# Performance work log

Hardware: AMD Instinct MI355X
Metric: run time of the kernel (lower is better)

## Reference

```python
import jax, jax.numpy as jnp
import numpy as np

H = 128        # hidden_channels
R = 32         # num_rbf
L = 2          # num_layers
CUTOFF = 4.5   # cutoff_upper (cutoff_lower = 0)
N_ATOMS = 2048
N_EDGES = 32768


def _tensor_norm(t):
    # Frobenius norm squared over the trailing 3x3 -> [N, H]
    return jnp.sum(t * t, axis=(-2, -1))


def _decompose(t):
    # Split into isotropic (I), antisymmetric (A), traceless symmetric (S) parts.
    eye = jnp.eye(3, dtype=t.dtype)
    I = (jnp.trace(t, axis1=-2, axis2=-1) / 3.0)[..., None, None] * eye
    A = 0.5 * (t - jnp.swapaxes(t, -2, -1))
    S = 0.5 * (t + jnp.swapaxes(t, -2, -1)) - I
    return I, A, S


def _chan_mix(T, W):
    # torch nn.Linear(H, H, bias=False) applied on the channel axis of [N,H,3,3]
    return jnp.einsum('nhij,gh->ngij', T, W)


def _interaction(X, edge_index, edge_weight, edge_attr, q,
                 W1, b1, W2, b2, W3, b3, Wt):
    N = X.shape[0]
    src, dst = edge_index[0], edge_index[1]
    # cosine cutoff (cutoff_lower = 0)
    C = 0.5 * (jnp.cos(edge_weight * (jnp.pi / CUTOFF)) + 1.0)
    C = C * (edge_weight < CUTOFF).astype(C.dtype)
    # edge scalar MLP: R -> H -> 2H -> 3H, silu
    ea = jax.nn.silu(edge_attr @ W1.T + b1)
    ea = jax.nn.silu(ea @ W2.T + b2)
    ea = jax.nn.silu(ea @ W3.T + b3)
    ea = (ea * C[:, None]).reshape(-1, H, 3)       # [E, H, 3]
    # normalize node tensors
    X = X / (_tensor_norm(X) + 1.0)[..., None, None]
    I, A, S = _decompose(X)
    I = _chan_mix(I, Wt[0])
    A = _chan_mix(A, Wt[1])
    S = _chan_mix(S, Wt[2])
    Y = I + A + S
    # per-edge tensor messages (Im + Am + Sm fused before the scatter)
    msg = (ea[:, :, 0, None, None] * I[dst]
           + ea[:, :, 1, None, None] * A[dst]
           + ea[:, :, 2, None, None] * S[dst])   # [E, H, 3, 3]
    M = jax.ops.segment_sum(msg, src, num_segments=N)
    # O(3) group: symmetrized tensor product, scaled by charge factor
    AB = jnp.matmul(M, Y) + jnp.matmul(Y, M)
    I, A, S = _decompose((1.0 + 0.1 * q[:, None, None, None]) * AB)
    normp1 = (_tensor_norm(I + A + S) + 1.0)[..., None, None]
    I, A, S = I / normp1, A / normp1, S / normp1
    I = _chan_mix(I, Wt[3])
    A = _chan_mix(A, Wt[4])
    S = _chan_mix(S, Wt[5])
    dX = I + A + S
    return X + dX + (1.0 + 0.1 * q[:, None, None, None]) * jnp.matmul(dX, dX)


def setup_inputs() -> dict:
    key = jax.random.key(0)
    ks = jax.random.split(key, 10)
    N, E = N_ATOMS, N_EDGES
    X = jax.random.normal(ks[0], (N, H, 3, 3), jnp.float32)
    edge_index = jax.random.randint(ks[1], (2, E), 0, N, jnp.int32)
    edge_weight = jax.random.uniform(ks[2], (E,), jnp.float32, 0.1, CUTOFF)
    edge_attr = jax.random.normal(ks[3], (E, R), jnp.float32)
    q = jax.random.normal(ks[4], (N,), jnp.float32) * 0.1
    s = 0.05
    Ws1 = jax.random.normal(ks[5], (L, H, R), jnp.float32) * s
    bs1 = jnp.zeros((L, H), jnp.float32)
    Ws2 = jax.random.normal(ks[6], (L, 2 * H, H), jnp.float32) * s
    bs2 = jnp.zeros((L, 2 * H), jnp.float32)
    Ws3 = jax.random.normal(ks[7], (L, 3 * H, 2 * H), jnp.float32) * s
    bs3 = jnp.zeros((L, 3 * H), jnp.float32)
    Wt = jax.random.normal(ks[8], (L, 6, H, H), jnp.float32) * s
    return dict(X=X, edge_attr=edge_attr, edge_weight=edge_weight, q=q,
                Ws1=Ws1, bs1=bs1, Ws2=Ws2, bs2=bs2, Ws3=Ws3, bs3=bs3,
                Wt=Wt, edge_index=edge_index)


def reference(X, edge_attr, edge_weight, q, Ws1, bs1, Ws2, bs2, Ws3, bs3, Wt, edge_index):
    for l in range(L):
        X = _interaction(X, edge_index, edge_weight, edge_attr, q,
                         Ws1[l], bs1[l], Ws2[l], bs2[l], Ws3[l], bs3[l], Wt[l])
    return X
```

## Files before the change

### kernel.cpp

```cpp
#include <hip/hip_runtime.h>
#include <hip/hip_bf16.h>
#include <math.h>

#define H 128
#define R 32
#define NATOMS 2048
#define NEDGES 32768
#define NH (NATOMS * H)
#define NP 1152
#define CUTOFF_F 4.5f
#define PI_OVER_CUTOFF 0.6981317007977318f

typedef __bf16 bf16x8 __attribute__((ext_vector_type(8)));
typedef float f32x4 __attribute__((ext_vector_type(4)));
typedef short short8 __attribute__((ext_vector_type(8)));

__device__ __forceinline__ float silu_f(float x) {
    return x / (1.f + __expf(-x));
}
__device__ __forceinline__ float b2f(unsigned short u) {
    return __uint_as_float(((unsigned)u) << 16);
}
__device__ __forceinline__ unsigned short f2b(float f) {
    __hip_bfloat16 h = __float2bfloat16(f);
    return __builtin_bit_cast(unsigned short, h);
}

__device__ __forceinline__ void build_full(const float d[9], float m[9]) {
    float i0 = d[0], a01 = d[1], a02 = d[2], a12 = d[3];
    float s00 = d[4], s01 = d[5], s02 = d[6], s11 = d[7], s12 = d[8];
    float s22 = -(s00 + s11);
    m[0] = i0 + s00;  m[1] = a01 + s01;  m[2] = a02 + s02;
    m[3] = s01 - a01; m[4] = i0 + s11;   m[5] = a12 + s12;
    m[6] = s02 - a02; m[7] = s12 - a12;  m[8] = i0 + s22;
}

#define C0 (NEDGES * R)
#define C1 (2 * H * R)
#define C2 (2 * 2 * H * H)
#define C3 (2 * 3 * H * 2 * H)
#define C4 (2 * 6 * H * H)
__global__ __launch_bounds__(256) void k_cast_all(
        const float* __restrict__ ea, const float* __restrict__ w1,
        const float* __restrict__ w2, const float* __restrict__ w3,
        const float* __restrict__ wt,
        __hip_bfloat16* __restrict__ oea, __hip_bfloat16* __restrict__ ow1,
        __hip_bfloat16* __restrict__ ow2, __hip_bfloat16* __restrict__ ow3,
        __hip_bfloat16* __restrict__ owt) {
    int i = blockIdx.x * 256 + threadIdx.x;
    if (i < C0) { oea[i] = __float2bfloat16(ea[i]); return; }
    i -= C0;
    if (i < C1) { ow1[i] = __float2bfloat16(w1[i]); return; }
    i -= C1;
    if (i < C2) { ow2[i] = __float2bfloat16(w2[i]); return; }
    i -= C2;
    if (i < C3) { ow3[i] = __float2bfloat16(w3[i]); return; }
    i -= C3;
    if (i < C4) { owt[i] = __float2bfloat16(wt[i]); }
}

__global__ __launch_bounds__(256) void k_node_prep(
        const float* __restrict__ X, float* __restrict__ Xn,
        __hip_bfloat16* __restrict__ Db) {
    int i = blockIdx.x * 256 + threadIdx.x;
    if (i >= NH) return;
    const float* x = X + (size_t)i * 9;
    float v[9];
    float ss = 0.f;
#pragma unroll
    for (int j = 0; j < 9; j++) { v[j] = x[j]; ss += v[j] * v[j]; }
    float inv = 1.f / (ss + 1.f);
#pragma unroll
    for (int j = 0; j < 9; j++) { v[j] *= inv; Xn[(size_t)i * 9 + j] = v[j]; }
    float i0 = (v[0] + v[4] + v[8]) * (1.f / 3.f);
    unsigned short* D = (unsigned short*)Db + (size_t)(i >> 7) * NP + (i & 127);
    D[0 * H] = f2b(i0);
    D[1 * H] = f2b(0.5f * (v[1] - v[3]));
    D[2 * H] = f2b(0.5f * (v[2] - v[6]));
    D[3 * H] = f2b(0.5f * (v[5] - v[7]));
    D[4 * H] = f2b(v[0] - i0);
    D[5 * H] = f2b(0.5f * (v[1] + v[3]));
    D[6 * H] = f2b(0.5f * (v[2] + v[6]));
    D[7 * H] = f2b(v[4] - i0);
    D[8 * H] = f2b(0.5f * (v[5] + v[7]));
}

struct TGm {
    static constexpr int BKm = 64;
    static constexpr int RB  = 128;
    static constexpr int SWZ = 7;
    static constexpr int NIT = 2;
    static constexpr int ABYTES = 128 * RB;
    static constexpr int BBYTES = 64 * RB;
    static constexpr int AISS = ABYTES / 4096;
    static constexpr int BISS = BBYTES / 4096;
    static constexpr int LDSB = ABYTES + BBYTES;
};

__device__ __forceinline__ void tile_gemm_mix(
        const __hip_bfloat16* __restrict__ A, int strideA,
        const __hip_bfloat16* __restrict__ W,
        int m0, int n0, char* lds, f32x4 acc[4][2]) {
    using T = TGm;
    const int t = threadIdx.x;
    const int lane = t & 63;
    const int w = t >> 6;

    auto stage = [&](int b, int it) {
        const int k0 = it * T::BKm;
        char* As = lds + b * T::LDSB;
        char* Bs = As + T::ABYTES;
#pragma unroll
        for (int i = 0; i < T::AISS; i++) {
            int base = (w * T::AISS + i) * 1024;
            int lin = base + lane * 16;
            int row = lin / T::RB;
            int slot = (lin % T::RB) >> 4;
            int sl = slot ^ (row & T::SWZ);
            const char* src = (const char*)(A + (size_t)(m0 + row) * strideA + k0) + sl * 16;
            __builtin_amdgcn_global_load_lds(
                (const __attribute__((address_space(1))) void*)src,
                (__attribute__((address_space(3))) void*)(As + base), 16, 0, 0);
        }
#pragma unroll
        for (int i = 0; i < T::BISS; i++) {
            int base = (w * T::BISS + i) * 1024;
            int lin = base + lane * 16;
            int row = lin / T::RB;
            int slot = (lin % T::RB) >> 4;
            int sl = slot ^ (row & T::SWZ);
            const char* src = (const char*)(W + (size_t)(n0 + row) * H + k0) + sl * 16;
            __builtin_amdgcn_global_load_lds(
                (const __attribute__((address_space(1))) void*)src,
                (__attribute__((address_space(3))) void*)(Bs + base), 16, 0, 0);
        }
    };

    auto compute = [&](int b) {
        const char* As = lds + b * T::LDSB;
        const char* Bs = As + T::ABYTES;
        const int wm = (w & 1) * 64;
        const int wn = (w >> 1) * 32;
        const int rA = wm + (lane & 15);
        const int rB = wn + (lane & 15);
        const int c = lane >> 4;
#pragma unroll
        for (int kk = 0; kk < T::BKm / 32; kk++) {
            bf16x8 av[4], bv[2];
#pragma unroll
            for (int mf = 0; mf < 4; mf++) {
                int row = rA + mf * 16;
                int sp = (kk * 4 + c) ^ (row & T::SWZ);
                av[mf] = __builtin_bit_cast(bf16x8,
                    *(const short8*)(As + row * T::RB + sp * 16));
            }
#pragma unroll
            for (int nf = 0; nf < 2; nf++) {
                int row = rB + nf * 16;
                int sp = (kk * 4 + c) ^ (row & T::SWZ);
                bv[nf] = __builtin_bit_cast(bf16x8,
                    *(const short8*)(Bs + row * T::RB + sp * 16));
            }
#pragma unroll
            for (int mf = 0; mf < 4; mf++)
#pragma unroll
                for (int nf = 0; nf < 2; nf++)
                    acc[mf][nf] = __builtin_amdgcn_mfma_f32_16x16x32_bf16(
                        av[mf], bv[nf], acc[mf][nf], 0, 0, 0);
        }
    };

    stage(0, 0);
    asm volatile("s_waitcnt vmcnt(0)" ::: "memory");
    __syncthreads();
    for (int it = 0; it < T::NIT; it++) {
        int b = it & 1;
        if (it + 1 < T::NIT) stage(b ^ 1, it + 1);
        compute(b);
        asm volatile("s_waitcnt vmcnt(0)" ::: "memory");
        __syncthreads();
    }
}

__global__ __launch_bounds__(256) void k_mix(
        const __hip_bfloat16* __restrict__ Db, const __hip_bfloat16* __restrict__ Wtb,
        __hip_bfloat16* __restrict__ Outp, int partOff) {
    __shared__ char lds[2 * TGm::LDSB];
    int c = blockIdx.z;
    int part = (c == 0) ? 0 : ((c < 4) ? 1 : 2);
    const __hip_bfloat16* A = Db + (size_t)c * H;
    const __hip_bfloat16* W = Wtb + (size_t)(partOff + part) * H * H;
    unsigned short* Out = (unsigned short*)Outp + (size_t)c * H;
    const int lane = threadIdx.x & 63;
    const int w = threadIdx.x >> 6;
    const int wm = (w & 1) * 64, wn = (w >> 1) * 32;
    const int m0 = blockIdx.x * 128, n0 = blockIdx.y * 64;
    f32x4 acc[4][2] = {};
    tile_gemm_mix(A, NP, W, m0, n0, lds, acc);
#pragma unroll
    for (int mf = 0; mf < 4; mf++)
#pragma unroll
        for (int r = 0; r < 4; r++) {
            int row = m0 + wm + mf * 16 + (lane >> 4) * 4 + r;
#pragma unroll
            for (int nf = 0; nf < 2; nf++) {
                int col = n0 + wn + nf * 16 + (lane & 15);
                Out[(size_t)row * NP + col] = f2b(acc[mf][nf][r]);
            }
        }
}

#define ETILE 64
#define PAD0 40
#define PAD1 136
#define PAD2 264
#define SA2_B (64 * PAD2 * 2)
#define SA1_B (64 * PAD1 * 2)

__global__ __launch_bounds__(256, 3) void k_mlp_fused(
        const __hip_bfloat16* __restrict__ eaB,
        const __hip_bfloat16* __restrict__ W1b, const __hip_bfloat16* __restrict__ W2b,
        const __hip_bfloat16* __restrict__ W3b,
        const float* __restrict__ bs1, const float* __restrict__ bs2,
        const float* __restrict__ bs3, const float* __restrict__ ew,
        __hip_bfloat16* __restrict__ ea3g) {
    const int l = blockIdx.z;
    const __hip_bfloat16* W1 = W1b + (size_t)l * (H * R);
    const __hip_bfloat16* W2 = W2b + (size_t)l * (2 * H * H);
    const __hip_bfloat16* W3 = W3b + (size_t)l * (3 * H * 2 * H);
    const float* b1 = bs1 + (size_t)l * H;
    const float* b2 = bs2 + (size_t)l * 2 * H;
    const float* b3 = bs3 + (size_t)l * 3 * H;
    unsigned short* outp = (unsigned short*)ea3g + (size_t)l * NEDGES * 384;
    const int e0 = blockIdx.x * ETILE;

    __shared__ char smem[SA2_B + SA1_B + 256 + 16];
    unsigned short* sA2 = (unsigned short*)smem;
    unsigned short* sEA = (unsigned short*)smem;
    unsigned short* sA1 = (unsigned short*)(smem + SA2_B);
    float* sEW = (float*)(smem + SA2_B + SA1_B);

    const int t = threadIdx.x;
    const int lane = t & 63;
    const int w = t >> 6;
    const int q = lane >> 4;
    const int li = lane & 15;

    {
        int row = t >> 2, c8 = t & 3;
        *(uint4*)(sEA + row * PAD0 + c8 * 8) =
            *(const uint4*)((const unsigned short*)eaB + (size_t)(e0 + row) * R + c8 * 8);
        if (t < ETILE) sEW[t] = ew[e0 + t];
    }
    __syncthreads();

    {
        f32x4 acc1[4][2] = {};
        bf16x8 bv[2];
#pragma unroll
        for (int nf = 0; nf < 2; nf++) {
            int col = w * 32 + nf * 16 + li;
            bv[nf] = __builtin_bit_cast(bf16x8,
                *(const short8*)((const unsigned short*)W1 + (size_t)col * R + q * 8));
        }
#pragma unroll
        for (int mf = 0; mf < 4; mf++) {
            int row = mf * 16 + li;
            bf16x8 av = __builtin_bit_cast(bf16x8,
                *(const short8*)(sEA + row * PAD0 + q * 8));
#pragma unroll
            for (int nf = 0; nf < 2; nf++)
                acc1[mf][nf] = __builtin_amdgcn_mfma_f32_16x16x32_bf16(
                    av, bv[nf], acc1[mf][nf], 0, 0, 0);
        }
        float bb[2];
#pragma unroll
        for (int nf = 0; nf < 2; nf++) bb[nf] = b1[w * 32 + nf * 16 + li];
        __syncthreads();
#pragma unroll
        for (int mf = 0; mf < 4; mf++)
#pragma unroll
            for (int r = 0; r < 4; r++) {
                int row = mf * 16 + q * 4 + r;
#pragma unroll
                for (int nf = 0; nf < 2; nf++) {
                    int col = w * 32 + nf * 16 + li;
                    sA1[row * PAD1 + col] = f2b(silu_f(acc1[mf][nf][r] + bb[nf]));
                }
            }
    }
    __syncthreads();

    {
        f32x4 acc2[4][4] = {};
#pragma unroll
        for (int ks = 0; ks < 4; ks++) {
            bf16x8 bv[4];
#pragma unroll
            for (int nf = 0; nf < 4; nf++) {
                int col = w * 64 + nf * 16 + li;
                bv[nf] = __builtin_bit_cast(bf16x8,
                    *(const short8*)((const unsigned short*)W2 + (size_t)col * H + ks * 32 + q * 8));
            }
#pragma unroll
            for (int mf = 0; mf < 4; mf++) {
                int row = mf * 16 + li;
                bf16x8 av = __builtin_bit_cast(bf16x8,
                    *(const short8*)(sA1 + row * PAD1 + ks * 32 + q * 8));
#pragma unroll
                for (int nf = 0; nf < 4; nf++)
                    acc2[mf][nf] = __builtin_amdgcn_mfma_f32_16x16x32_bf16(
                        av, bv[nf], acc2[mf][nf], 0, 0, 0);
            }
        }
        float bb[4];
#pragma unroll
        for (int nf = 0; nf < 4; nf++) bb[nf] = b2[w * 64 + nf * 16 + li];
        __syncthreads();
#pragma unroll
        for (int mf = 0; mf < 4; mf++)
#pragma unroll
            for (int r = 0; r < 4; r++) {
                int row = mf * 16 + q * 4 + r;
#pragma unroll
                for (int nf = 0; nf < 4; nf++) {
                    int col = w * 64 + nf * 16 + li;
                    sA2[row * PAD2 + col] = f2b(silu_f(acc2[mf][nf][r] + bb[nf]));
                }
            }
    }
    __syncthreads();

    {
        f32x4 acc3[4][6] = {};
#pragma unroll
        for (int ks = 0; ks < 8; ks++) {
            bf16x8 bv[6];
#pragma unroll
            for (int nf = 0; nf < 6; nf++) {
                int col = w * 96 + nf * 16 + li;
                bv[nf] = __builtin_bit_cast(bf16x8,
                    *(const short8*)((const unsigned short*)W3 + (size_t)col * (2 * H) + ks * 32 + q * 8));
            }
#pragma unroll
            for (int mf = 0; mf < 4; mf++) {
                int row = mf * 16 + li;
                bf16x8 av = __builtin_bit_cast(bf16x8,
                    *(const short8*)(sA2 + row * PAD2 + ks * 32 + q * 8));
#pragma unroll
                for (int nf = 0; nf < 6; nf++)
                    acc3[mf][nf] = __builtin_amdgcn_mfma_f32_16x16x32_bf16(
                        av, bv[nf], acc3[mf][nf], 0, 0, 0);
            }
        }
        float bb[6];
#pragma unroll
        for (int nf = 0; nf < 6; nf++) bb[nf] = b3[w * 96 + nf * 16 + li];
#pragma unroll
        for (int mf = 0; mf < 4; mf++)
#pragma unroll
            for (int r = 0; r < 4; r++) {
                int row = mf * 16 + q * 4 + r;
                float wv = sEW[row];
                float cs = (wv < CUTOFF_F) ? 0.5f * (__cosf(wv * PI_OVER_CUTOFF) + 1.f) : 0.f;
#pragma unroll
                for (int nf = 0; nf < 6; nf++) {
                    int col = w * 96 + nf * 16 + li;
                    float x = silu_f(acc3[mf][nf][r] + bb[nf]) * cs;
                    outp[(size_t)(e0 + row) * 384 + col] = f2b(x);
                }
            }
    }
}

__global__ __launch_bounds__(256) void k_hist(
        const int* __restrict__ eidx, int* __restrict__ cnt) {
    int e = blockIdx.x * 256 + threadIdx.x;
    if (e < NEDGES) atomicAdd(&cnt[eidx[e]], 1);
}

__global__ __launch_bounds__(256) void k_scan(
        const int* __restrict__ cnt, int* __restrict__ rowstart,
        int* __restrict__ cursor) {
    __shared__ int partial[256];
    int t = threadIdx.x;
    int loc[8];
    int run = 0;
#pragma unroll
    for (int j = 0; j < 8; j++) {
        int v = cnt[t * 8 + j];
        loc[j] = run; run += v;
    }
    partial[t] = run;
    __syncthreads();
    if (t == 0) {
        int acc = 0;
        for (int i = 0; i < 256; i++) { int v = partial[i]; partial[i] = acc; acc += v; }
        rowstart[2048] = acc;
    }
    __syncthreads();
    int base = partial[t];
#pragma unroll
    for (int j = 0; j < 8; j++) {
        rowstart[t * 8 + j] = base + loc[j];
        cursor[t * 8 + j] = base + loc[j];
    }
}

__global__ __launch_bounds__(256) void k_fill(
        const int* __restrict__ eidx, int* __restrict__ cursor,
        int* __restrict__ elist) {
    int e = blockIdx.x * 256 + threadIdx.x;
    if (e >= NEDGES) return;
    int src = eidx[e];
    int pos = atomicAdd(&cursor[src], 1);
    elist[pos] = e;
}

__global__ __launch_bounds__(256) void k_gather_ab(
        const __hip_bfloat16* __restrict__ ea,
        const int* __restrict__ eidx,
        const int* __restrict__ rowstart, const int* __restrict__ elist,
        const __hip_bfloat16* __restrict__ Yb, const float* __restrict__ q,
        __hip_bfloat16* __restrict__ Tb) {
    int gid = blockIdx.x * 256 + threadIdx.x;
    int n = gid >> 6;
    int h0 = (gid & 63) << 1;
    int beg = rowstart[n], end = rowstart[n + 1];
    const unsigned short* Y = (const unsigned short*)Yb;
    float acc[9][2];
#pragma unroll
    for (int c = 0; c < 9; c++) { acc[c][0] = 0.f; acc[c][1] = 0.f; }
    for (int idx = beg; idx < end; ++idx) {
        int e = elist[idx];
        int dst = eidx[NEDGES + e];
        const unsigned short* eap = (const unsigned short*)ea + (size_t)e * 384 + h0 * 3;
        unsigned u0 = *(const unsigned*)(eap);
        unsigned u1 = *(const unsigned*)(eap + 2);
        unsigned u2 = *(const unsigned*)(eap + 4);
        float w0a = b2f(u0 & 0xffff), w1a = b2f(u0 >> 16);
        float w2a = b2f(u1 & 0xffff), w0b = b2f(u1 >> 16);
        float w1b = b2f(u2 & 0xffff), w2b = b2f(u2 >> 16);
        const unsigned short* yp = Y + (size_t)dst * NP + h0;
        ushort2 y;
        y = *(const ushort2*)(yp + 0 * H); acc[0][0] += w0a * b2f(y.x); acc[0][1] += w0b * b2f(y.y);
        y = *(const ushort2*)(yp + 1 * H); acc[1][0] += w1a * b2f(y.x); acc[1][1] += w1b * b2f(y.y);
        y = *(const ushort2*)(yp + 2 * H); acc[2][0] += w1a * b2f(y.x); acc[2][1] += w1b * b2f(y.y);
        y = *(const ushort2*)(yp + 3 * H); acc[3][0] += w1a * b2f(y.x); acc[3][1] += w1b * b2f(y.y);
#pragma unroll
        for (int c = 4; c < 9; c++) {
            y = *(const ushort2*)(yp + c * H);
            acc[c][0] += w2a * b2f(y.x); acc[c][1] += w2b * b2f(y.y);
        }
    }
    const unsigned short* yp = Y + (size_t)n * NP + h0;
    float scale = 1.f + 0.1f * q[n];
    float yd2[9][2];
#pragma unroll
    for (int c = 0; c < 9; c++) {
        ushort2 y = *(const ushort2*)(yp + (size_t)c * H);
        yd2[c][0] = b2f(y.x); yd2[c][1] = b2f(y.y);
    }
    unsigned short outw[9][2];
#pragma unroll
    for (int col = 0; col < 2; col++) {
        float md[9], yd[9];
#pragma unroll
        for (int c = 0; c < 9; c++) { md[c] = acc[c][col]; yd[c] = yd2[c][col]; }
        float m[9], yf[9];
        build_full(md, m);
        build_full(yd, yf);
        float ab[9];
#pragma unroll
        for (int ii = 0; ii < 3; ii++)
#pragma unroll
            for (int jj = 0; jj < 3; jj++) {
                float s = 0.f;
#pragma unroll
                for (int kk = 0; kk < 3; kk++)
                    s += m[ii * 3 + kk] * yf[kk * 3 + jj] + yf[ii * 3 + kk] * m[kk * 3 + jj];
                ab[ii * 3 + jj] = s;
            }
        float nrm = 0.f;
#pragma unroll
        for (int j = 0; j < 9; j++) { ab[j] *= scale; nrm += ab[j] * ab[j]; }
        float inv = 1.f / (nrm + 1.f);
        float tr3 = (ab[0] + ab[4] + ab[8]) * (1.f / 3.f);
        outw[0][col] = f2b(tr3 * inv);
        outw[1][col] = f2b(0.5f * (ab[1] - ab[3]) * inv);
        outw[2][col] = f2b(0.5f * (ab[2] - ab[6]) * inv);
        outw[3][col] = f2b(0.5f * (ab[5] - ab[7]) * inv);
        outw[4][col] = f2b((ab[0] - tr3) * inv);
        outw[5][col] = f2b(0.5f * (ab[1] + ab[3]) * inv);
        outw[6][col] = f2b(0.5f * (ab[2] + ab[6]) * inv);
        outw[7][col] = f2b((ab[4] - tr3) * inv);
        outw[8][col] = f2b(0.5f * (ab[5] + ab[7]) * inv);
    }
    unsigned short* T = (unsigned short*)Tb + (size_t)n * NP + h0;
#pragma unroll
    for (int c = 0; c < 9; c++) {
        ushort2 o; o.x = outw[c][0]; o.y = outw[c][1];
        *(ushort2*)(T + (size_t)c * H) = o;
    }
}

template <bool PREP>
__global__ __launch_bounds__(256) void k_final(
        const __hip_bfloat16* __restrict__ dXb, const float* __restrict__ Xn,
        const float* __restrict__ q, float* __restrict__ Xout,
        float* __restrict__ XnW, __hip_bfloat16* __restrict__ Db) {
    int i = blockIdx.x * 256 + threadIdx.x;
    if (i >= NH) return;
    const unsigned short* dX = (const unsigned short*)dXb + (size_t)(i >> 7) * NP + (i & 127);
    float dd[9];
#pragma unroll
    for (int c = 0; c < 9; c++) dd[c] = b2f(dX[(size_t)c * H]);
    float dx[9];
    build_full(dd, dx);
    float scale = 1.f + 0.1f * q[i >> 7];
    float out[9];
#pragma unroll
    for (int ii = 0; ii < 3; ii++)
#pragma unroll
        for (int jj = 0; jj < 3; jj++) {
            float s = 0.f;
#pragma unroll
            for (int kk = 0; kk < 3; kk++)
                s += dx[ii * 3 + kk] * dx[kk * 3 + jj];
            out[ii * 3 + jj] = Xn[(size_t)i * 9 + ii * 3 + jj] + dx[ii * 3 + jj] + scale * s;
        }
#pragma unroll
    for (int j = 0; j < 9; j++) Xout[(size_t)i * 9 + j] = out[j];
    if (PREP) {
        float ss = 0.f;
#pragma unroll
        for (int j = 0; j < 9; j++) ss += out[j] * out[j];
        float inv = 1.f / (ss + 1.f);
        float v[9];
#pragma unroll
        for (int j = 0; j < 9; j++) { v[j] = out[j] * inv; XnW[(size_t)i * 9 + j] = v[j]; }
        float i0 = (v[0] + v[4] + v[8]) * (1.f / 3.f);
        unsigned short* D = (unsigned short*)Db + (size_t)(i >> 7) * NP + (i & 127);
        D[0 * H] = f2b(i0);
        D[1 * H] = f2b(0.5f * (v[1] - v[3]));
        D[2 * H] = f2b(0.5f * (v[2] - v[6]));
        D[3 * H] = f2b(0.5f * (v[5] - v[7]));
        D[4 * H] = f2b(v[0] - i0);
        D[5 * H] = f2b(0.5f * (v[1] + v[3]));
        D[6 * H] = f2b(0.5f * (v[2] + v[6]));
        D[7 * H] = f2b(v[4] - i0);
        D[8 * H] = f2b(0.5f * (v[5] + v[7]));
    }
}

extern "C" void kernel_launch(void* const* d_in, const int* in_sizes, int n_in,
                              void* d_out, int out_size, void* d_ws, size_t ws_size,
                              hipStream_t stream) {
    const float* X          = (const float*)d_in[0];
    const float* edge_attr  = (const float*)d_in[1];
    const float* edge_weight= (const float*)d_in[2];
    const float* q          = (const float*)d_in[3];
    const float* Ws1        = (const float*)d_in[4];
    const float* bs1        = (const float*)d_in[5];
    const float* Ws2        = (const float*)d_in[6];
    const float* bs2        = (const float*)d_in[7];
    const float* Ws3        = (const float*)d_in[8];
    const float* bs3        = (const float*)d_in[9];
    const float* Wt         = (const float*)d_in[10];
    const int*   eidx       = (const int*)d_in[11];
    float* Xout = (float*)d_out;

    char* p = (char*)d_ws;
    auto alloc = [&](size_t bytes) -> char* {
        char* r = p; p += (bytes + 255) & ~(size_t)255; return r;
    };
    size_t nodeBytes = (size_t)NH * 9 * sizeof(float);
    float* Xn   = (float*)alloc(nodeBytes);
    __hip_bfloat16* Db = (__hip_bfloat16*)alloc((size_t)NH * 9 * 2);
    __hip_bfloat16* Yb = (__hip_bfloat16*)alloc((size_t)NH * 9 * 2);
    __hip_bfloat16* eaB = (__hip_bfloat16*)alloc((size_t)C0 * 2);
    __hip_bfloat16* W1b = (__hip_bfloat16*)alloc((size_t)C1 * 2);
    __hip_bfloat16* W2b = (__hip_bfloat16*)alloc((size_t)C2 * 2);
    __hip_bfloat16* W3b = (__hip_bfloat16*)alloc((size_t)C3 * 2);
    __hip_bfloat16* Wtb = (__hip_bfloat16*)alloc((size_t)C4 * 2);
    __hip_bfloat16* ea3g = (__hip_bfloat16*)alloc((size_t)2 * NEDGES * 384 * 2);
    int* cnt      = (int*)alloc(2048 * 4);
    int* rowstart = (int*)alloc(2049 * 4);
    int* cursor   = (int*)alloc(2048 * 4);
    int* elist    = (int*)alloc(NEDGES * 4);

    k_cast_all<<<(C0 + C1 + C2 + C3 + C4) / 256, 256, 0, stream>>>(
        edge_attr, Ws1, Ws2, Ws3, Wt, eaB, W1b, W2b, W3b, Wtb);

    hipMemsetAsync(cnt, 0, 2048 * sizeof(int), stream);
    k_hist<<<NEDGES / 256, 256, 0, stream>>>(eidx, cnt);
    k_scan<<<1, 256, 0, stream>>>(cnt, rowstart, cursor);
    k_fill<<<NEDGES / 256, 256, 0, stream>>>(eidx, cursor, elist);

    k_node_prep<<<NH / 256, 256, 0, stream>>>(X, Xn, Db);

    k_mlp_fused<<<dim3(NEDGES / ETILE, 1, 2), 256, 0, stream>>>(
        eaB, W1b, W2b, W3b, bs1, bs2, bs3, edge_weight, ea3g);

    for (int l = 0; l < 2; l++) {
        const __hip_bfloat16* Wtl = Wtb + (size_t)l * 6 * H * H;
        const __hip_bfloat16* ea3 = ea3g + (size_t)l * NEDGES * 384;

        k_mix<<<dim3(NATOMS / 128, 2, 9), 256, 0, stream>>>(Db, Wtl, Yb, 0);
        k_gather_ab<<<NH / 512, 256, 0, stream>>>(
            ea3, eidx, rowstart, elist, Yb, q, Db);
        k_mix<<<dim3(NATOMS / 128, 2, 9), 256, 0, stream>>>(Db, Wtl, Yb, 3);
        if (l == 0)
            k_final<true><<<NH / 256, 256, 0, stream>>>(Yb, Xn, q, Xout, Xn, Db);
        else
            k_final<false><<<NH / 256, 256, 0, stream>>>(Yb, Xn, q, Xout, nullptr, nullptr);
    }
}
```

Baseline: 177.2 us.

## Prefetch MLP weight fragments, split layer-3 N tiles, and double gather threads

```diff
diff --git a/kernel.cpp b/kernel.cpp
--- a/kernel.cpp
+++ b/kernel.cpp
@@ -225,9 +225,9 @@
         const float* __restrict__ bs3, const float* __restrict__ ew,
         __hip_bfloat16* __restrict__ ea3g) {
     const int l = blockIdx.z;
-    const __hip_bfloat16* W1 = W1b + (size_t)l * (H * R);
-    const __hip_bfloat16* W2 = W2b + (size_t)l * (2 * H * H);
-    const __hip_bfloat16* W3 = W3b + (size_t)l * (3 * H * 2 * H);
+    const unsigned short* W1 = (const unsigned short*)W1b + (size_t)l * (H * R);
+    const unsigned short* W2 = (const unsigned short*)W2b + (size_t)l * (2 * H * H);
+    const unsigned short* W3 = (const unsigned short*)W3b + (size_t)l * (3 * H * 2 * H);
     const float* b1 = bs1 + (size_t)l * H;
     const float* b2 = bs2 + (size_t)l * 2 * H;
     const float* b3 = bs3 + (size_t)l * 3 * H;
@@ -261,7 +261,7 @@
         for (int nf = 0; nf < 2; nf++) {
             int col = w * 32 + nf * 16 + li;
             bv[nf] = __builtin_bit_cast(bf16x8,
-                *(const short8*)((const unsigned short*)W1 + (size_t)col * R + q * 8));
+                *(const short8*)(W1 + (size_t)col * R + q * 8));
         }
 #pragma unroll
         for (int mf = 0; mf < 4; mf++) {
@@ -293,25 +293,34 @@
 
     {
         f32x4 acc2[4][4] = {};
+        bf16x8 b2v[2][4];
+#pragma unroll
+        for (int nf = 0; nf < 4; nf++)
+            b2v[0][nf] = __builtin_bit_cast(bf16x8,
+                *(const short8*)(W2 + (size_t)(w * 64 + nf * 16 + li) * H + q * 8));
 #pragma unroll
         for (int ks = 0; ks < 4; ks++) {
-            bf16x8 bv[4];
-#pragma unroll
-            for (int nf = 0; nf < 4; nf++) {
-                int col = w * 64 + nf * 16 + li;
-                bv[nf] = __builtin_bit_cast(bf16x8,
-                    *(const short8*)((const unsigned short*)W2 + (size_t)col * H + ks * 32 + q * 8));
-            }
-#pragma unroll
-            for (int mf = 0; mf < 4; mf++) {
-                int row = mf * 16 + li;
-                bf16x8 av = __builtin_bit_cast(bf16x8,
-                    *(const short8*)(sA1 + row * PAD1 + ks * 32 + q * 8));
+            const int cur = ks & 1;
+            if (ks < 3) {
+#pragma unroll
+                for (int nf = 0; nf < 4; nf++)
+                    b2v[cur ^ 1][nf] = __builtin_bit_cast(bf16x8,
+                        *(const short8*)(W2 + (size_t)(w * 64 + nf * 16 + li) * H
+                                         + (ks + 1) * 32 + q * 8));
+            }
+            bf16x8 av[4];
+#pragma unroll
+            for (int mf = 0; mf < 4; mf++)
+                av[mf] = __builtin_bit_cast(bf16x8,
+                    *(const short8*)(sA1 + (mf * 16 + li) * PAD1 + ks * 32 + q * 8));
+            __builtin_amdgcn_s_setprio(1);
+#pragma unroll
+            for (int mf = 0; mf < 4; mf++)
 #pragma unroll
                 for (int nf = 0; nf < 4; nf++)
                     acc2[mf][nf] = __builtin_amdgcn_mfma_f32_16x16x32_bf16(
-                        av, bv[nf], acc2[mf][nf], 0, 0, 0);
-            }
+                        av[mf], b2v[cur][nf], acc2[mf][nf], 0, 0, 0);
+            __builtin_amdgcn_s_setprio(0);
         }
         float bb[4];
 #pragma unroll
@@ -331,31 +340,42 @@
     }
     __syncthreads();
 
-    {
-        f32x4 acc3[4][6] = {};
+#pragma unroll
+    for (int hn = 0; hn < 2; hn++) {
+        const int cbase = w * 96 + hn * 48;
+        f32x4 acc3[4][3] = {};
+        bf16x8 b3v[2][3];
+#pragma unroll
+        for (int nf = 0; nf < 3; nf++)
+            b3v[0][nf] = __builtin_bit_cast(bf16x8,
+                *(const short8*)(W3 + (size_t)(cbase + nf * 16 + li) * (2 * H) + q * 8));
 #pragma unroll
         for (int ks = 0; ks < 8; ks++) {
-            bf16x8 bv[6];
-#pragma unroll
-            for (int nf = 0; nf < 6; nf++) {
-                int col = w * 96 + nf * 16 + li;
-                bv[nf] = __builtin_bit_cast(bf16x8,
-                    *(const short8*)((const unsigned short*)W3 + (size_t)col * (2 * H) + ks * 32 + q * 8));
-            }
-#pragma unroll
-            for (int mf = 0; mf < 4; mf++) {
-                int row = mf * 16 + li;
-                bf16x8 av = __builtin_bit_cast(bf16x8,
-                    *(const short8*)(sA2 + row * PAD2 + ks * 32 + q * 8));
-#pragma unroll
-                for (int nf = 0; nf < 6; nf++)
+            const int cur = ks & 1;
+            if (ks < 7) {
+#pragma unroll
+                for (int nf = 0; nf < 3; nf++)
+                    b3v[cur ^ 1][nf] = __builtin_bit_cast(bf16x8,
+                        *(const short8*)(W3 + (size_t)(cbase + nf * 16 + li) * (2 * H)
+                                         + (ks + 1) * 32 + q * 8));
+            }
+            bf16x8 av[4];
+#pragma unroll
+            for (int mf = 0; mf < 4; mf++)
+                av[mf] = __builtin_bit_cast(bf16x8,
+                    *(const short8*)(sA2 + (mf * 16 + li) * PAD2 + ks * 32 + q * 8));
+            __builtin_amdgcn_s_setprio(1);
+#pragma unroll
+            for (int mf = 0; mf < 4; mf++)
+#pragma unroll
+                for (int nf = 0; nf < 3; nf++)
                     acc3[mf][nf] = __builtin_amdgcn_mfma_f32_16x16x32_bf16(
-                        av, bv[nf], acc3[mf][nf], 0, 0, 0);
-            }
-        }
-        float bb[6];
-#pragma unroll
-        for (int nf = 0; nf < 6; nf++) bb[nf] = b3[w * 96 + nf * 16 + li];
+                        av[mf], b3v[cur][nf], acc3[mf][nf], 0, 0, 0);
+            __builtin_amdgcn_s_setprio(0);
+        }
+        float bb[3];
+#pragma unroll
+        for (int nf = 0; nf < 3; nf++) bb[nf] = b3[cbase + nf * 16 + li];
 #pragma unroll
         for (int mf = 0; mf < 4; mf++)
 #pragma unroll
@@ -364,8 +384,8 @@
                 float wv = sEW[row];
                 float cs = (wv < CUTOFF_F) ? 0.5f * (__cosf(wv * PI_OVER_CUTOFF) + 1.f) : 0.f;
 #pragma unroll
-                for (int nf = 0; nf < 6; nf++) {
-                    int col = w * 96 + nf * 16 + li;
+                for (int nf = 0; nf < 3; nf++) {
+                    int col = cbase + nf * 16 + li;
                     float x = silu_f(acc3[mf][nf][r] + bb[nf]) * cs;
                     outp[(size_t)(e0 + row) * 384 + col] = f2b(x);
                 }
@@ -418,20 +438,23 @@
 }
 
 __global__ __launch_bounds__(256) void k_gather_ab(
-        const __hip_bfloat16* __restrict__ ea,
+        const __hip_bfloat16* __restrict__ ea ,
         const int* __restrict__ eidx,
         const int* __restrict__ rowstart, const int* __restrict__ elist,
         const __hip_bfloat16* __restrict__ Yb, const float* __restrict__ q,
         __hip_bfloat16* __restrict__ Tb) {
     int gid = blockIdx.x * 256 + threadIdx.x;
-    int n = gid >> 6;
-    int h0 = (gid & 63) << 1;
+    int n = gid >> 7;
+    int t7 = gid & 127;
+    int hp = t7 >> 1;
+    int half = t7 & 1;
+    int h0 = hp << 1;
     int beg = rowstart[n], end = rowstart[n + 1];
     const unsigned short* Y = (const unsigned short*)Yb;
     float acc[9][2];
 #pragma unroll
     for (int c = 0; c < 9; c++) { acc[c][0] = 0.f; acc[c][1] = 0.f; }
-    for (int idx = beg; idx < end; ++idx) {
+    for (int idx = beg + half; idx < end; idx += 2) {
         int e = elist[idx];
         int dst = eidx[NEDGES + e];
         const unsigned short* eap = (const unsigned short*)ea + (size_t)e * 384 + h0 * 3;
@@ -453,55 +476,49 @@
             acc[c][0] += w2a * b2f(y.x); acc[c][1] += w2b * b2f(y.y);
         }
     }
-    const unsigned short* yp = Y + (size_t)n * NP + h0;
+#pragma unroll
+    for (int c = 0; c < 9; c++) {
+        acc[c][0] += __shfl_xor(acc[c][0], 1);
+        acc[c][1] += __shfl_xor(acc[c][1], 1);
+    }
+    int hcol = h0 + half;
+    const unsigned short* yp = Y + (size_t)n * NP + hcol;
     float scale = 1.f + 0.1f * q[n];
-    float yd2[9][2];
+    float md[9], yd[9];
 #pragma unroll
     for (int c = 0; c < 9; c++) {
-        ushort2 y = *(const ushort2*)(yp + (size_t)c * H);
-        yd2[c][0] = b2f(y.x); yd2[c][1] = b2f(y.y);
-    }
-    unsigned short outw[9][2];
-#pragma unroll
-    for (int col = 0; col < 2; col++) {
-        float md[9], yd[9];
-#pragma unroll
-        for (int c = 0; c < 9; c++) { md[c] = acc[c][col]; yd[c] = yd2[c][col]; }
-        float m[9], yf[9];
-        build_full(md, m);
-        build_full(yd, yf);
-        float ab[9];
-#pragma unroll
-        for (int ii = 0; ii < 3; ii++)
-#pragma unroll
-            for (int jj = 0; jj < 3; jj++) {
-                float s = 0.f;
-#pragma unroll
-                for (int kk = 0; kk < 3; kk++)
-                    s += m[ii * 3 + kk] * yf[kk * 3 + jj] + yf[ii * 3 + kk] * m[kk * 3 + jj];
-                ab[ii * 3 + jj] = s;
-            }
-        float nrm = 0.f;
-#pragma unroll
-        for (int j = 0; j < 9; j++) { ab[j] *= scale; nrm += ab[j] * ab[j]; }
-        float inv = 1.f / (nrm + 1.f);
-        float tr3 = (ab[0] + ab[4] + ab[8]) * (1.f / 3.f);
-        outw[0][col] = f2b(tr3 * inv);
-        outw[1][col] = f2b(0.5f * (ab[1] - ab[3]) * inv);
-        outw[2][col] = f2b(0.5f * (ab[2] - ab[6]) * inv);
-        outw[3][col] = f2b(0.5f * (ab[5] - ab[7]) * inv);
-        outw[4][col] = f2b((ab[0] - tr3) * inv);
-        outw[5][col] = f2b(0.5f * (ab[1] + ab[3]) * inv);
-        outw[6][col] = f2b(0.5f * (ab[2] + ab[6]) * inv);
-        outw[7][col] = f2b((ab[4] - tr3) * inv);
-        outw[8][col] = f2b(0.5f * (ab[5] + ab[7]) * inv);
-    }
-    unsigned short* T = (unsigned short*)Tb + (size_t)n * NP + h0;
-#pragma unroll
-    for (int c = 0; c < 9; c++) {
-        ushort2 o; o.x = outw[c][0]; o.y = outw[c][1];
-        *(ushort2*)(T + (size_t)c * H) = o;
-    }
+        md[c] = acc[c][half];
+        yd[c] = b2f(yp[(size_t)c * H]);
+    }
+    float m[9], yf[9];
+    build_full(md, m);
+    build_full(yd, yf);
+    float ab[9];
+#pragma unroll
+    for (int ii = 0; ii < 3; ii++)
+#pragma unroll
+        for (int jj = 0; jj < 3; jj++) {
+            float s = 0.f;
+#pragma unroll
+            for (int kk = 0; kk < 3; kk++)
+                s += m[ii * 3 + kk] * yf[kk * 3 + jj] + yf[ii * 3 + kk] * m[kk * 3 + jj];
+            ab[ii * 3 + jj] = s;
+        }
+    float nrm = 0.f;
+#pragma unroll
+    for (int j = 0; j < 9; j++) { ab[j] *= scale; nrm += ab[j] * ab[j]; }
+    float inv = 1.f / (nrm + 1.f);
+    float tr3 = (ab[0] + ab[4] + ab[8]) * (1.f / 3.f);
+    unsigned short* T = (unsigned short*)Tb + (size_t)n * NP + hcol;
+    T[0 * H] = f2b(tr3 * inv);
+    T[1 * H] = f2b(0.5f * (ab[1] - ab[3]) * inv);
+    T[2 * H] = f2b(0.5f * (ab[2] - ab[6]) * inv);
+    T[3 * H] = f2b(0.5f * (ab[5] - ab[7]) * inv);
+    T[4 * H] = f2b((ab[0] - tr3) * inv);
+    T[5 * H] = f2b(0.5f * (ab[1] + ab[3]) * inv);
+    T[6 * H] = f2b(0.5f * (ab[2] + ab[6]) * inv);
+    T[7 * H] = f2b((ab[4] - tr3) * inv);
+    T[8 * H] = f2b(0.5f * (ab[5] + ab[7]) * inv);
 }
 
 template <bool PREP>
@@ -607,7 +624,7 @@
         const __hip_bfloat16* ea3 = ea3g + (size_t)l * NEDGES * 384;
 
         k_mix<<<dim3(NATOMS / 128, 2, 9), 256, 0, stream>>>(Db, Wtl, Yb, 0);
-        k_gather_ab<<<NH / 512, 256, 0, stream>>>(
+        k_gather_ab<<<NH / 256, 256, 0, stream>>>(
             ea3, eidx, rowstart, elist, Yb, q, Db);
         k_mix<<<dim3(NATOMS / 128, 2, 9), 256, 0, stream>>>(Db, Wtl, Yb, 3);
         if (l == 0)
```

Measured after the change: 166.4 us. -6.1%, faster.
